# Optimization experiments

Hardware: AMD Instinct MI355X
Metric: run time of the kernel (lower is better)

The kernel has to match this reference:

```python
import jax, jax.numpy as jnp
import numpy as np

B, S, D = 2, 4096, 1024
H = 16
HD = D // H  # head_dim = 64

def setup_inputs() -> dict:
    key = jax.random.key(0)
    ks = jax.random.split(key, 9)
    sc = 1.0 / np.sqrt(D)
    return {
        "X":   jax.random.normal(ks[0], (B, S, D), dtype=jnp.float32),
        "Wq":  jax.random.normal(ks[1], (D, D), dtype=jnp.float32) * sc,
        "bq":  jax.random.normal(ks[2], (D,), dtype=jnp.float32) * 0.01,
        "Wk":  jax.random.normal(ks[3], (D, D), dtype=jnp.float32) * sc,
        "bk":  jax.random.normal(ks[4], (D,), dtype=jnp.float32) * 0.01,
        "Wv":  jax.random.normal(ks[5], (D, D), dtype=jnp.float32) * sc,
        "bv":  jax.random.normal(ks[6], (D,), dtype=jnp.float32) * 0.01,
        "Wo":  jax.random.normal(ks[7], (D, D), dtype=jnp.float32) * sc,
        "bo":  jax.random.normal(ks[8], (D,), dtype=jnp.float32) * 0.01,
    }

def reference(X, Wq, bq, Wk, bk, Wv, bv, Wo, bo):
    b, s, d = X.shape
    h, hd = H, HD
    # projections
    Q = X @ Wq + bq
    K = X @ Wk + bk
    V = X @ Wv + bv
    # [b, h, s, hd]
    Q = Q.reshape(b, s, h, hd).transpose(0, 2, 1, 3)
    K = K.reshape(b, s, h, hd).transpose(0, 2, 1, 3)
    V = V.reshape(b, s, h, hd).transpose(0, 2, 1, 3)
    scale = 1.0 / jnp.sqrt(jnp.asarray(hd, dtype=X.dtype))  # sqrt(hidden/num_heads)
    scores = jnp.einsum("bhqd,bhkd->bhqk", Q, K) * scale
    attn = jax.nn.softmax(scores, axis=-1)
    out = jnp.einsum("bhqk,bhkd->bhqd", attn, V)
    out = out.transpose(0, 2, 1, 3).reshape(b, s, d)
    return out @ Wo + bo
```

## Files before the change

kernel.cpp:

```cpp
#include <hip/hip_runtime.h>

#define Bsz 2
#define Sq  4096
#define Dm  1024
#define NH  16
#define HD  64

typedef __attribute__((ext_vector_type(8))) short short8;
typedef __attribute__((ext_vector_type(4))) float f32x4;
typedef __attribute__((ext_vector_type(2))) __fp16 fp16x2;
typedef __attribute__((ext_vector_type(4))) _Float16 half4v;
typedef __attribute__((ext_vector_type(8))) _Float16 half8v;

__device__ __forceinline__ unsigned short f2bf(float x) {
    unsigned int u = __float_as_uint(x);
    u += 0x7fffu + ((u >> 16) & 1u);
    return (unsigned short)(u >> 16);
}

__device__ __forceinline__ void gl2lds16(const unsigned short* g, unsigned short* l) {
    __builtin_amdgcn_global_load_lds(
        (const __attribute__((address_space(1))) unsigned int*)g,
        (__attribute__((address_space(3))) unsigned int*)l, 16, 0, 0);
}

__global__ __launch_bounds__(256) void cvt_bf16(const float4* __restrict__ in,
                                                ushort4* __restrict__ out) {
    const int i = blockIdx.x * 256 + threadIdx.x;
    const float4 v = in[i];
    ushort4 r;
    r.x = f2bf(v.x); r.y = f2bf(v.y); r.z = f2bf(v.z); r.w = f2bf(v.w);
    out[i] = r;
}

__global__ __launch_bounds__(256) void wtrans4(const float* __restrict__ Wq,
                                               const float* __restrict__ Wk,
                                               const float* __restrict__ Wv,
                                               const float* __restrict__ Wo,
                                               unsigned short* __restrict__ WtAll) {
    __shared__ float tile[64][65];
    const int z = blockIdx.z;
    const float* W = (z == 0) ? Wq : (z == 1) ? Wk : (z == 2) ? Wv : Wo;
    unsigned short* Wt = WtAll + (size_t)z * Dm * Dm;
    const int k0 = blockIdx.y * 64, n0 = blockIdx.x * 64;
    const int t = threadIdx.x;
    #pragma unroll
    for (int i = 0; i < 16; ++i) {
        const int idx = t + i * 256, r = idx >> 6, c = idx & 63;
        tile[r][c] = W[(size_t)(k0 + r) * Dm + n0 + c];
    }
    __syncthreads();
    #pragma unroll
    for (int i = 0; i < 16; ++i) {
        const int idx = t + i * 256, rr = idx >> 6, cc = idx & 63;
        Wt[(size_t)(n0 + rr) * Dm + k0 + cc] = f2bf(tile[cc][rr]);
    }
}

struct GemmCtx {
    int wm, wn, quad, c16;
    f32x4 acc[4][4];
};

__device__ __forceinline__ void gemm_core(
    const unsigned short* __restrict__ A,
    const unsigned short* __restrict__ Bt,
    int bm, int bn, unsigned short* As, unsigned short* Bs, GemmCtx& cx)
{
    const int t    = threadIdx.x;
    const int w    = t >> 6;
    const int lane = t & 63;
    cx.quad = lane >> 4;
    cx.c16  = lane & 15;
    cx.wm = (w >> 1) * 64;
    cx.wn = (w & 1) * 64;

    #pragma unroll
    for (int i = 0; i < 4; ++i)
        #pragma unroll
        for (int j = 0; j < 4; ++j)
            cx.acc[i][j] = (f32x4){0.f, 0.f, 0.f, 0.f};

    const int srow = lane >> 2, soff = (lane & 3) * 8;
    const unsigned short* Ag0 = A  + (size_t)(bm + w * 16 + srow) * Dm + soff;
    const unsigned short* Ag1 = Ag0 + (size_t)64 * Dm;
    const unsigned short* Bg0 = Bt + (size_t)(bn + w * 16 + srow) * Dm + soff;
    const unsigned short* Bg1 = Bg0 + (size_t)64 * Dm;
    unsigned short* Al0 = As + (w * 16) * 32;
    unsigned short* Al1 = As + (64 + w * 16) * 32;
    unsigned short* Bl0 = Bs + (w * 16) * 32;
    unsigned short* Bl1 = Bs + (64 + w * 16) * 32;

    for (int k0 = 0; k0 < Dm; k0 += 32) {
        __syncthreads();
        gl2lds16(Ag0 + k0, Al0);
        gl2lds16(Ag1 + k0, Al1);
        gl2lds16(Bg0 + k0, Bl0);
        gl2lds16(Bg1 + k0, Bl1);
        __syncthreads();

        short8 af[4], bf[4];
        #pragma unroll
        for (int mt = 0; mt < 4; ++mt)
            af[mt] = *(const short8*)(As + (cx.wm + mt * 16 + cx.c16) * 32 + cx.quad * 8);
        #pragma unroll
        for (int nt = 0; nt < 4; ++nt)
            bf[nt] = *(const short8*)(Bs + (cx.wn + nt * 16 + cx.c16) * 32 + cx.quad * 8);
        #pragma unroll
        for (int mt = 0; mt < 4; ++mt)
            #pragma unroll
            for (int nt = 0; nt < 4; ++nt)
                cx.acc[mt][nt] = __builtin_amdgcn_mfma_f32_16x16x32_bf16(
                    af[mt], bf[nt], cx.acc[mt][nt], 0, 0, 0);
    }
}

__global__ __launch_bounds__(256) void gemm_qkv(
    const unsigned short* __restrict__ A,
    const unsigned short* __restrict__ WtAll,
    const float* __restrict__ bq, const float* __restrict__ bk,
    const float* __restrict__ bv,
    unsigned short* __restrict__ Qh, unsigned short* __restrict__ Kh,
    unsigned short* __restrict__ Vt, float qscale)
{
    __shared__ unsigned short As[128 * 32];
    __shared__ unsigned short Bs[128 * 32];
    const int bm = blockIdx.y * 128;
    const int bn = blockIdx.x * 128;
    GemmCtx cx;
    gemm_core(A, WtAll, bm, bn, As, Bs, cx);

    const int which = bn >> 10;
    const float* bias = (which == 0) ? bq : (which == 1) ? bk : bv;
    const float osc = (which == 0) ? qscale : 1.0f;

    #pragma unroll
    for (int mt = 0; mt < 4; ++mt) {
        const int m0 = bm + cx.wm + mt * 16 + cx.quad * 4;
        #pragma unroll
        for (int nt = 0; nt < 4; ++nt) {
            const int n  = bn + cx.wn + nt * 16 + cx.c16;
            const int nl = n & 1023;
            const float bvv = bias[nl];
            const int h = (nl >> 6), d = nl & 63;
            if (which < 2) {
                unsigned short* C = (which == 0) ? Qh : Kh;
                #pragma unroll
                for (int r = 0; r < 4; ++r) {
                    const int m = m0 + r;
                    const int b = m >> 12, s = m & (Sq - 1);
                    C[((size_t)(b * NH + h) * Sq + s) * HD + d] =
                        f2bf((cx.acc[mt][nt][r] + bvv) * osc);
                }
            } else {
                const int b = m0 >> 12, s0 = m0 & (Sq - 1);
                union { fp16x2 h2[2]; unsigned int u[2]; } pk;
                pk.h2[0] = __builtin_amdgcn_cvt_pkrtz(cx.acc[mt][nt][0] + bvv,
                                                      cx.acc[mt][nt][1] + bvv);
                pk.h2[1] = __builtin_amdgcn_cvt_pkrtz(cx.acc[mt][nt][2] + bvv,
                                                      cx.acc[mt][nt][3] + bvv);
                *(uint2*)(Vt + ((size_t)(b * NH + h) * HD + d) * Sq + s0) =
                    make_uint2(pk.u[0], pk.u[1]);
            }
        }
    }
}

__global__ __launch_bounds__(256) void gemm_o(
    const unsigned short* __restrict__ A,
    const unsigned short* __restrict__ Bt,
    const float* __restrict__ bias, float* __restrict__ C)
{
    __shared__ unsigned short As[128 * 32];
    __shared__ unsigned short Bs[128 * 32];
    const int bm = blockIdx.y * 128;
    const int bn = blockIdx.x * 128;
    GemmCtx cx;
    gemm_core(A, Bt, bm, bn, As, Bs, cx);

    #pragma unroll
    for (int mt = 0; mt < 4; ++mt) {
        const int m0 = bm + cx.wm + mt * 16 + cx.quad * 4;
        #pragma unroll
        for (int nt = 0; nt < 4; ++nt) {
            const int n = bn + cx.wn + nt * 16 + cx.c16;
            const float bvv = bias[n];
            #pragma unroll
            for (int r = 0; r < 4; ++r)
                C[(size_t)(m0 + r) * Dm + n] = cx.acc[mt][nt][r] + bvv;
        }
    }
}

__global__ __launch_bounds__(256, 2) void attn_mfma6(
    const unsigned short* __restrict__ Q,
    const unsigned short* __restrict__ K,
    const unsigned short* __restrict__ Vt,
    unsigned short* __restrict__ AO)
{
    __shared__ unsigned short Ks[2][64 * 64];
    __shared__ unsigned short Vs[2][64 * 64];

    const int qt = blockIdx.x;
    const int bh = blockIdx.y;
    const int b = bh >> 4, h = bh & 15;
    const int t    = threadIdx.x;
    const int w    = t >> 6;
    const int lane = t & 63;
    const int quad = lane >> 4;
    const int c16  = lane & 15;
    const size_t base = (size_t)bh * Sq * HD;

    short8 qf[4][2];
    #pragma unroll
    for (int qg = 0; qg < 4; ++qg) {
        const unsigned short* qp =
            Q + base + (size_t)(qt * 256 + w * 64 + qg * 16 + c16) * HD;
        qf[qg][0] = *(const short8*)(qp + quad * 8);
        qf[qg][1] = *(const short8*)(qp + 32 + quad * 8);
    }

    f32x4 O[4][4];
    f32x4 Lsum[4];
    #pragma unroll
    for (int qg = 0; qg < 4; ++qg) {
        Lsum[qg] = (f32x4){0.f, 0.f, 0.f, 0.f};
        #pragma unroll
        for (int g = 0; g < 4; ++g)
            O[qg][g] = (f32x4){0.f, 0.f, 0.f, 0.f};
    }
    half8v ones8;
    #pragma unroll
    for (int i = 0; i < 8; ++i) ones8[i] = (_Float16)1.f;

    const int srow = t >> 2, sc4 = (t & 3) * 8;
    const int swr = (srow & 7) << 3;
    const int f0 = (sc4 < 16) ? sc4 * 2 : (sc4 - 16) * 2 + 4;
    const int f1 = (sc4 + 4 < 16) ? (sc4 + 4) * 2 : (sc4 - 12) * 2 + 4;
    const int kc0 = sc4 ^ swr, kc1 = (sc4 + 32) ^ swr;
    const int vc0 = f0 ^ swr, vc1 = f1 ^ swr;
    const int vc2 = (32 + f0) ^ swr, vc3 = (32 + f1) ^ swr;

    const unsigned short* kg = K  + base + (size_t)srow * HD + sc4;
    const unsigned short* vg = Vt + base + (size_t)srow * Sq + sc4;
    unsigned short* ksl = &Ks[0][0] + srow * 64;
    unsigned short* vsl = &Vs[0][0] + srow * 64;
    const int LBUF = 64 * 64;

    int4 kr0, kr1, vr0, vr1;
    kr0 = *(const int4*)(kg);
    kr1 = *(const int4*)(kg + 32);
    vr0 = *(const int4*)(vg);
    vr1 = *(const int4*)(vg + 32);
    *(int4*)(ksl + kc0) = kr0;
    *(int4*)(ksl + kc1) = kr1;
    *(uint2*)(vsl + vc0) = make_uint2(vr0.x, vr0.y);
    *(uint2*)(vsl + vc1) = make_uint2(vr0.z, vr0.w);
    *(uint2*)(vsl + vc2) = make_uint2(vr1.x, vr1.y);
    *(uint2*)(vsl + vc3) = make_uint2(vr1.z, vr1.w);

    for (int kt = 0; kt < Sq / 64; ++kt) {
        const int cur = kt & 1;
        if (kt + 1 < Sq / 64) {
            const unsigned short* kp = kg + (size_t)(kt + 1) * 64 * HD;
            const unsigned short* vp = vg + (kt + 1) * 64;
            kr0 = *(const int4*)(kp);
            kr1 = *(const int4*)(kp + 32);
            vr0 = *(const int4*)(vp);
            vr1 = *(const int4*)(vp + 32);
        }
        __syncthreads();

        const unsigned short* ksb = &Ks[cur][0];
        const unsigned short* vsb = &Vs[cur][0];

        half4v P4[4][4];
        #pragma unroll
        for (int nt = 0; nt < 4; ++nt) {
            const int krow = nt * 16 + c16;
            const int ksw = (krow & 7) << 3;
            const short8 kf0 = *(const short8*)(ksb + krow * 64 + ((quad * 8) ^ ksw));
            const short8 kf1 = *(const short8*)(ksb + krow * 64 + ((32 + quad * 8) ^ ksw));
            #pragma unroll
            for (int qg = 0; qg < 4; ++qg) {
                f32x4 z = (f32x4){0.f, 0.f, 0.f, 0.f};
                z = __builtin_amdgcn_mfma_f32_16x16x32_bf16(kf0, qf[qg][0], z, 0, 0, 0);
                z = __builtin_amdgcn_mfma_f32_16x16x32_bf16(kf1, qf[qg][1], z, 0, 0, 0);
                const float p0 = __builtin_amdgcn_exp2f(z[0]);
                const float p1 = __builtin_amdgcn_exp2f(z[1]);
                const float p2 = __builtin_amdgcn_exp2f(z[2]);
                const float p3 = __builtin_amdgcn_exp2f(z[3]);
                union { fp16x2 h2[2]; half4v h4; } pk;
                pk.h2[0] = __builtin_amdgcn_cvt_pkrtz(p0, p1);
                pk.h2[1] = __builtin_amdgcn_cvt_pkrtz(p2, p3);
                P4[qg][nt] = pk.h4;
            }
        }

        half8v P32[4][2];
        #pragma unroll
        for (int qg = 0; qg < 4; ++qg) {
            #pragma unroll
            for (int cc = 0; cc < 2; ++cc) {
                union { half4v h4[2]; half8v h8; } u;
                u.h4[0] = P4[qg][2 * cc];
                u.h4[1] = P4[qg][2 * cc + 1];
                P32[qg][cc] = u.h8;
            }
        }

        #pragma unroll
        for (int cc = 0; cc < 2; ++cc) {
            #pragma unroll
            for (int g = 0; g < 4; ++g) {
                const int vrow = g * 16 + c16;
                const half8v vf = *(const half8v*)
                    (vsb + vrow * 64 + ((cc * 32 + quad * 8) ^ ((vrow & 7) << 3)));
                #pragma unroll
                for (int qg = 0; qg < 4; ++qg)
                    O[qg][g] = __builtin_amdgcn_mfma_f32_16x16x32_f16(
                        P32[qg][cc], vf, O[qg][g], 0, 0, 0);
            }
            #pragma unroll
            for (int qg = 0; qg < 4; ++qg)
                Lsum[qg] = __builtin_amdgcn_mfma_f32_16x16x32_f16(
                    P32[qg][cc], ones8, Lsum[qg], 0, 0, 0);
        }

        if (kt + 1 < Sq / 64) {
            const int nb = cur ^ 1;
            *(int4*)(ksl + nb * LBUF + kc0) = kr0;
            *(int4*)(ksl + nb * LBUF + kc1) = kr1;
            unsigned short* vdst = vsl + nb * LBUF;
            *(uint2*)(vdst + vc0) = make_uint2(vr0.x, vr0.y);
            *(uint2*)(vdst + vc1) = make_uint2(vr0.z, vr0.w);
            *(uint2*)(vdst + vc2) = make_uint2(vr1.x, vr1.y);
            *(uint2*)(vdst + vc3) = make_uint2(vr1.z, vr1.w);
        }
    }

    #pragma unroll
    for (int qg = 0; qg < 4; ++qg) {
        float linv[4];
        #pragma unroll
        for (int r = 0; r < 4; ++r) linv[r] = 1.f / Lsum[qg][r];
        #pragma unroll
        for (int g = 0; g < 4; ++g) {
            const int col = h * HD + g * 16 + c16;
            #pragma unroll
            for (int r = 0; r < 4; ++r) {
                const int s = qt * 256 + w * 64 + qg * 16 + quad * 4 + r;
                AO[((size_t)(b * Sq + s)) * Dm + col] = f2bf(O[qg][g][r] * linv[r]);
            }
        }
    }
}

extern "C" void kernel_launch(void* const* d_in, const int* in_sizes, int n_in,
                              void* d_out, int out_size, void* d_ws, size_t ws_size,
                              hipStream_t stream)
{
    const float* X  = (const float*)d_in[0];
    const float* Wq = (const float*)d_in[1];
    const float* bq = (const float*)d_in[2];
    const float* Wk = (const float*)d_in[3];
    const float* bk = (const float*)d_in[4];
    const float* Wv = (const float*)d_in[5];
    const float* bv = (const float*)d_in[6];
    const float* Wo = (const float*)d_in[7];
    const float* bo = (const float*)d_in[8];
    float* out = (float*)d_out;

    unsigned short* ws = (unsigned short*)d_ws;
    const size_t NX = (size_t)Bsz * Sq * Dm;
    const size_t NW = (size_t)Dm * Dm;
    unsigned short* Xb    = ws; ws += NX;
    unsigned short* WtAll = ws; ws += 4 * NW;
    unsigned short* Qh    = ws; ws += NX;
    unsigned short* Kh    = ws; ws += NX;
    unsigned short* Vt    = ws; ws += NX;
    unsigned short* AO    = ws; ws += NX;

    cvt_bf16<<<(int)(NX / 1024), 256, 0, stream>>>((const float4*)X, (ushort4*)Xb);
    wtrans4<<<dim3(16, 16, 4), 256, 0, stream>>>(Wq, Wk, Wv, Wo, WtAll);

    const float SCL = 0.18033688011112042f;
    gemm_qkv<<<dim3(3 * Dm / 128, (Bsz * Sq) / 128), 256, 0, stream>>>(
        Xb, WtAll, bq, bk, bv, Qh, Kh, Vt, SCL);

    attn_mfma6<<<dim3(Sq / 256, Bsz * NH), 256, 0, stream>>>(Qh, Kh, Vt, AO);

    gemm_o<<<dim3(Dm / 128, (Bsz * Sq) / 128), 256, 0, stream>>>(
        AO, WtAll + 3 * NW, bo, out);
}
```

Measured before the change: 319.0 us.

## Halve attention query tile, raise occupancy, remap grid, add MFMA priority hints

The attention kernel now covers 128 query rows per workgroup instead of 256, which doubles the grid to 1024 workgroups. Launch bounds rise to 4 blocks per CU, and a 1D block index is remapped so neighbouring workgroups are spread across heads, likely to balance L2 reuse of K/V across XCDs. s_setprio raises wave priority around the MFMA sections so matrix work from one wave can overlap exp work from others. Each K/V tile loaded into LDS is now reused by fewer queries, so total K/V traffic doubles in exchange for more waves to hide latency.

```diff
diff --git a/kernel.cpp b/kernel.cpp
--- a/kernel.cpp
+++ b/kernel.cpp
@@ -192,7 +192,7 @@
     }
 }
 
-__global__ __launch_bounds__(256, 2) void attn_mfma6(
+__global__ __launch_bounds__(256, 4) void attn_mfma7(
     const unsigned short* __restrict__ Q,
     const unsigned short* __restrict__ K,
     const unsigned short* __restrict__ Vt,
@@ -201,8 +201,10 @@
     __shared__ unsigned short Ks[2][64 * 64];
     __shared__ unsigned short Vs[2][64 * 64];
 
-    const int qt = blockIdx.x;
-    const int bh = blockIdx.y;
+    const int wg  = blockIdx.x;
+    const int j   = wg >> 3;
+    const int bh  = (wg & 7) * 4 + (j >> 5);
+    const int qt  = j & 31;
     const int b = bh >> 4, h = bh & 15;
     const int t    = threadIdx.x;
     const int w    = t >> 6;
@@ -211,19 +213,19 @@
     const int c16  = lane & 15;
     const size_t base = (size_t)bh * Sq * HD;
 
-    short8 qf[4][2];
-    #pragma unroll
-    for (int qg = 0; qg < 4; ++qg) {
+    short8 qf[2][2];
+    #pragma unroll
+    for (int qg = 0; qg < 2; ++qg) {
         const unsigned short* qp =
-            Q + base + (size_t)(qt * 256 + w * 64 + qg * 16 + c16) * HD;
+            Q + base + (size_t)(qt * 128 + w * 32 + qg * 16 + c16) * HD;
         qf[qg][0] = *(const short8*)(qp + quad * 8);
         qf[qg][1] = *(const short8*)(qp + 32 + quad * 8);
     }
 
-    f32x4 O[4][4];
-    f32x4 Lsum[4];
-    #pragma unroll
-    for (int qg = 0; qg < 4; ++qg) {
+    f32x4 O[2][4];
+    f32x4 Lsum[2];
+    #pragma unroll
+    for (int qg = 0; qg < 2; ++qg) {
         Lsum[qg] = (f32x4){0.f, 0.f, 0.f, 0.f};
         #pragma unroll
         for (int g = 0; g < 4; ++g)
@@ -274,22 +276,28 @@
         const unsigned short* ksb = &Ks[cur][0];
         const unsigned short* vsb = &Vs[cur][0];
 
-        half4v P4[4][4];
+        half4v P4[2][4];
         #pragma unroll
         for (int nt = 0; nt < 4; ++nt) {
             const int krow = nt * 16 + c16;
             const int ksw = (krow & 7) << 3;
             const short8 kf0 = *(const short8*)(ksb + krow * 64 + ((quad * 8) ^ ksw));
             const short8 kf1 = *(const short8*)(ksb + krow * 64 + ((32 + quad * 8) ^ ksw));
-            #pragma unroll
-            for (int qg = 0; qg < 4; ++qg) {
-                f32x4 z = (f32x4){0.f, 0.f, 0.f, 0.f};
-                z = __builtin_amdgcn_mfma_f32_16x16x32_bf16(kf0, qf[qg][0], z, 0, 0, 0);
-                z = __builtin_amdgcn_mfma_f32_16x16x32_bf16(kf1, qf[qg][1], z, 0, 0, 0);
-                const float p0 = __builtin_amdgcn_exp2f(z[0]);
-                const float p1 = __builtin_amdgcn_exp2f(z[1]);
-                const float p2 = __builtin_amdgcn_exp2f(z[2]);
-                const float p3 = __builtin_amdgcn_exp2f(z[3]);
+            f32x4 z[2];
+            __builtin_amdgcn_s_setprio(1);
+            #pragma unroll
+            for (int qg = 0; qg < 2; ++qg) {
+                z[qg] = (f32x4){0.f, 0.f, 0.f, 0.f};
+                z[qg] = __builtin_amdgcn_mfma_f32_16x16x32_bf16(kf0, qf[qg][0], z[qg], 0, 0, 0);
+                z[qg] = __builtin_amdgcn_mfma_f32_16x16x32_bf16(kf1, qf[qg][1], z[qg], 0, 0, 0);
+            }
+            __builtin_amdgcn_s_setprio(0);
+            #pragma unroll
+            for (int qg = 0; qg < 2; ++qg) {
+                const float p0 = __builtin_amdgcn_exp2f(z[qg][0]);
+                const float p1 = __builtin_amdgcn_exp2f(z[qg][1]);
+                const float p2 = __builtin_amdgcn_exp2f(z[qg][2]);
+                const float p3 = __builtin_amdgcn_exp2f(z[qg][3]);
                 union { fp16x2 h2[2]; half4v h4; } pk;
                 pk.h2[0] = __builtin_amdgcn_cvt_pkrtz(p0, p1);
                 pk.h2[1] = __builtin_amdgcn_cvt_pkrtz(p2, p3);
@@ -297,9 +305,9 @@
             }
         }
 
-        half8v P32[4][2];
-        #pragma unroll
-        for (int qg = 0; qg < 4; ++qg) {
+        half8v P32[2][2];
+        #pragma unroll
+        for (int qg = 0; qg < 2; ++qg) {
             #pragma unroll
             for (int cc = 0; cc < 2; ++cc) {
                 union { half4v h4[2]; half8v h8; } u;
@@ -309,6 +317,7 @@
             }
         }
 
+        __builtin_amdgcn_s_setprio(1);
         #pragma unroll
         for (int cc = 0; cc < 2; ++cc) {
             #pragma unroll
@@ -317,15 +326,16 @@
                 const half8v vf = *(const half8v*)
                     (vsb + vrow * 64 + ((cc * 32 + quad * 8) ^ ((vrow & 7) << 3)));
                 #pragma unroll
-                for (int qg = 0; qg < 4; ++qg)
+                for (int qg = 0; qg < 2; ++qg)
                     O[qg][g] = __builtin_amdgcn_mfma_f32_16x16x32_f16(
                         P32[qg][cc], vf, O[qg][g], 0, 0, 0);
             }
             #pragma unroll
-            for (int qg = 0; qg < 4; ++qg)
+            for (int qg = 0; qg < 2; ++qg)
                 Lsum[qg] = __builtin_amdgcn_mfma_f32_16x16x32_f16(
                     P32[qg][cc], ones8, Lsum[qg], 0, 0, 0);
         }
+        __builtin_amdgcn_s_setprio(0);
 
         if (kt + 1 < Sq / 64) {
             const int nb = cur ^ 1;
@@ -340,7 +350,7 @@
     }
 
     #pragma unroll
-    for (int qg = 0; qg < 4; ++qg) {
+    for (int qg = 0; qg < 2; ++qg) {
         float linv[4];
         #pragma unroll
         for (int r = 0; r < 4; ++r) linv[r] = 1.f / Lsum[qg][r];
@@ -349,7 +359,7 @@
             const int col = h * HD + g * 16 + c16;
             #pragma unroll
             for (int r = 0; r < 4; ++r) {
-                const int s = qt * 256 + w * 64 + qg * 16 + quad * 4 + r;
+                const int s = qt * 128 + w * 32 + qg * 16 + quad * 4 + r;
                 AO[((size_t)(b * Sq + s)) * Dm + col] = f2bf(O[qg][g][r] * linv[r]);
             }
         }
@@ -388,7 +398,7 @@
     gemm_qkv<<<dim3(3 * Dm / 128, (Bsz * Sq) / 128), 256, 0, stream>>>(
         Xb, WtAll, bq, bk, bv, Qh, Kh, Vt, SCL);
 
-    attn_mfma6<<<dim3(Sq / 256, Bsz * NH), 256, 0, stream>>>(Qh, Kh, Vt, AO);
+    attn_mfma7<<<dim3(32 * 32), 256, 0, stream>>>(Qh, Kh, Vt, AO);
 
     gemm_o<<<dim3(Dm / 128, (Bsz * Sq) / 128), 256, 0, stream>>>(
         AO, WtAll + 3 * NW, bo, out);
```

Measured after the change: 345.8 us. 1.08x slower.

## Software-pipeline QK MFMA with exp and remap attention grid for XCD locality

Applied to the files above, without the earlier changes.

Restructures the attention inner loop so the QK^T MFMAs for one 16-key slice are issued while the exp2/convert work of the previous slice runs. Sched barriers and s_setprio around the MFMA groups enforce that interleaving, and the K/V LDS stores for the next tile are split around the two PV steps. It also flattens the grid to one dimension and remaps block IDs so that consecutive blocks (wg & 7 selecting the XCD) map to a fixed set of batch-heads, aiming for better L2 reuse of K/V. The cost is more live registers for the z buffers, which could affect occupancy at 2 waves per SIMD.

```diff
diff --git a/kernel.cpp b/kernel.cpp
--- a/kernel.cpp
+++ b/kernel.cpp
@@ -192,7 +192,7 @@
     }
 }
 
-__global__ __launch_bounds__(256, 2) void attn_mfma6(
+__global__ __launch_bounds__(256, 2) void attn_mfma8(
     const unsigned short* __restrict__ Q,
     const unsigned short* __restrict__ K,
     const unsigned short* __restrict__ Vt,
@@ -201,8 +201,10 @@
     __shared__ unsigned short Ks[2][64 * 64];
     __shared__ unsigned short Vs[2][64 * 64];
 
-    const int qt = blockIdx.x;
-    const int bh = blockIdx.y;
+    const int wg  = blockIdx.x;
+    const int j   = wg >> 3;
+    const int bh  = (wg & 7) * 4 + (j >> 4);
+    const int qt  = j & 15;
     const int b = bh >> 4, h = bh & 15;
     const int t    = threadIdx.x;
     const int w    = t >> 6;
@@ -274,63 +276,83 @@
         const unsigned short* ksb = &Ks[cur][0];
         const unsigned short* vsb = &Vs[cur][0];
 
+        f32x4 z0[4], z1[4], z2[4], z3[4];
         half4v P4[4][4];
-        #pragma unroll
-        for (int nt = 0; nt < 4; ++nt) {
-            const int krow = nt * 16 + c16;
+
+        auto qkstep = [&](int nt5, f32x4* z) {
+            const int krow = nt5 * 16 + c16;
             const int ksw = (krow & 7) << 3;
             const short8 kf0 = *(const short8*)(ksb + krow * 64 + ((quad * 8) ^ ksw));
             const short8 kf1 = *(const short8*)(ksb + krow * 64 + ((32 + quad * 8) ^ ksw));
+            __builtin_amdgcn_s_setprio(1);
             #pragma unroll
             for (int qg = 0; qg < 4; ++qg) {
-                f32x4 z = (f32x4){0.f, 0.f, 0.f, 0.f};
-                z = __builtin_amdgcn_mfma_f32_16x16x32_bf16(kf0, qf[qg][0], z, 0, 0, 0);
-                z = __builtin_amdgcn_mfma_f32_16x16x32_bf16(kf1, qf[qg][1], z, 0, 0, 0);
-                const float p0 = __builtin_amdgcn_exp2f(z[0]);
-                const float p1 = __builtin_amdgcn_exp2f(z[1]);
-                const float p2 = __builtin_amdgcn_exp2f(z[2]);
-                const float p3 = __builtin_amdgcn_exp2f(z[3]);
+                f32x4 zz = (f32x4){0.f, 0.f, 0.f, 0.f};
+                zz = __builtin_amdgcn_mfma_f32_16x16x32_bf16(kf0, qf[qg][0], zz, 0, 0, 0);
+                zz = __builtin_amdgcn_mfma_f32_16x16x32_bf16(kf1, qf[qg][1], zz, 0, 0, 0);
+                z[qg] = zz;
+            }
+            __builtin_amdgcn_s_setprio(0);
+            __builtin_amdgcn_sched_barrier(0);
+        };
+        auto expstep = [&](const f32x4* z, half4v* Pn) {
+            #pragma unroll
+            for (int qg = 0; qg < 4; ++qg) {
+                const float p0 = __builtin_amdgcn_exp2f(z[qg][0]);
+                const float p1 = __builtin_amdgcn_exp2f(z[qg][1]);
+                const float p2 = __builtin_amdgcn_exp2f(z[qg][2]);
+                const float p3 = __builtin_amdgcn_exp2f(z[qg][3]);
                 union { fp16x2 h2[2]; half4v h4; } pk;
                 pk.h2[0] = __builtin_amdgcn_cvt_pkrtz(p0, p1);
                 pk.h2[1] = __builtin_amdgcn_cvt_pkrtz(p2, p3);
-                P4[qg][nt] = pk.h4;
-            }
-        }
-
-        half8v P32[4][2];
-        #pragma unroll
-        for (int qg = 0; qg < 4; ++qg) {
-            #pragma unroll
-            for (int cc = 0; cc < 2; ++cc) {
+                Pn[qg] = pk.h4;
+            }
+        };
+        auto pvstep = [&](int cc) {
+            half8v P32[4];
+            #pragma unroll
+            for (int qg = 0; qg < 4; ++qg) {
                 union { half4v h4[2]; half8v h8; } u;
-                u.h4[0] = P4[qg][2 * cc];
-                u.h4[1] = P4[qg][2 * cc + 1];
-                P32[qg][cc] = u.h8;
-            }
-        }
-
-        #pragma unroll
-        for (int cc = 0; cc < 2; ++cc) {
+                u.h4[0] = P4[2 * cc][qg];
+                u.h4[1] = P4[2 * cc + 1][qg];
+                P32[qg] = u.h8;
+            }
+            half8v vf[4];
             #pragma unroll
             for (int g = 0; g < 4; ++g) {
                 const int vrow = g * 16 + c16;
-                const half8v vf = *(const half8v*)
+                vf[g] = *(const half8v*)
                     (vsb + vrow * 64 + ((cc * 32 + quad * 8) ^ ((vrow & 7) << 3)));
+            }
+            __builtin_amdgcn_s_setprio(1);
+            #pragma unroll
+            for (int g = 0; g < 4; ++g)
                 #pragma unroll
                 for (int qg = 0; qg < 4; ++qg)
                     O[qg][g] = __builtin_amdgcn_mfma_f32_16x16x32_f16(
-                        P32[qg][cc], vf, O[qg][g], 0, 0, 0);
-            }
+                        P32[qg], vf[g], O[qg][g], 0, 0, 0);
             #pragma unroll
             for (int qg = 0; qg < 4; ++qg)
                 Lsum[qg] = __builtin_amdgcn_mfma_f32_16x16x32_f16(
-                    P32[qg][cc], ones8, Lsum[qg], 0, 0, 0);
-        }
-
+                    P32[qg], ones8, Lsum[qg], 0, 0, 0);
+            __builtin_amdgcn_s_setprio(0);
+            __builtin_amdgcn_sched_barrier(0);
+        };
+
+        qkstep(0, z0);
+        qkstep(1, z1);  expstep(z0, P4[0]);
+        qkstep(2, z2);  expstep(z1, P4[1]);
+        qkstep(3, z3);  expstep(z2, P4[2]);
+        pvstep(0);
+        expstep(z3, P4[3]);
         if (kt + 1 < Sq / 64) {
             const int nb = cur ^ 1;
             *(int4*)(ksl + nb * LBUF + kc0) = kr0;
             *(int4*)(ksl + nb * LBUF + kc1) = kr1;
+        }
+        pvstep(1);
+        if (kt + 1 < Sq / 64) {
+            const int nb = cur ^ 1;
             unsigned short* vdst = vsl + nb * LBUF;
             *(uint2*)(vdst + vc0) = make_uint2(vr0.x, vr0.y);
             *(uint2*)(vdst + vc1) = make_uint2(vr0.z, vr0.w);
@@ -388,7 +410,7 @@
     gemm_qkv<<<dim3(3 * Dm / 128, (Bsz * Sq) / 128), 256, 0, stream>>>(
         Xb, WtAll, bq, bk, bv, Qh, Kh, Vt, SCL);
 
-    attn_mfma6<<<dim3(Sq / 256, Bsz * NH), 256, 0, stream>>>(Qh, Kh, Vt, AO);
+    attn_mfma8<<<dim3(512), 256, 0, stream>>>(Qh, Kh, Vt, AO);
 
     gemm_o<<<dim3(Dm / 128, (Bsz * Sq) / 128), 256, 0, stream>>>(
         AO, WtAll + 3 * NW, bo, out);
```

Result: no change. 316.7 us (-0.7%).

## Async K loads to LDS, remap blocks across XCDs, and reorder MFMA with setprio

Applied to the files above, without the earlier changes.

The attention kernel now loads K tiles straight into LDS with global_load_lds, so K no longer passes through registers. The 1D grid is remapped so consecutive workgroups, which land on different XCDs, each take a different (batch, head), which should improve L2 reuse of K/V. The S=QK^T MFMAs are regrouped per K subtile, V fragments are prefetched, and the PV MFMAs are split in two halves around the V LDS store. s_setprio is added around MFMA bursts to encourage overlap across waves. The barrier moves to the top of the loop, which is still correct under double buffering but reorders the synchronisation.

```diff
diff --git a/kernel.cpp b/kernel.cpp
--- a/kernel.cpp
+++ b/kernel.cpp
@@ -192,7 +192,7 @@
     }
 }
 
-__global__ __launch_bounds__(256, 2) void attn_mfma6(
+__global__ __launch_bounds__(256, 2) void attn_mfma11(
     const unsigned short* __restrict__ Q,
     const unsigned short* __restrict__ K,
     const unsigned short* __restrict__ Vt,
@@ -201,8 +201,10 @@
     __shared__ unsigned short Ks[2][64 * 64];
     __shared__ unsigned short Vs[2][64 * 64];
 
-    const int qt = blockIdx.x;
-    const int bh = blockIdx.y;
+    const int wg  = blockIdx.x;
+    const int j   = wg >> 3;
+    const int bh  = (wg & 7) * 4 + (j >> 4);
+    const int qt  = j & 15;
     const int b = bh >> 4, h = bh & 15;
     const int t    = threadIdx.x;
     const int w    = t >> 6;
@@ -232,28 +234,27 @@
     half8v ones8;
     #pragma unroll
     for (int i = 0; i < 8; ++i) ones8[i] = (_Float16)1.f;
+    const f32x4 zero4 = (f32x4){0.f, 0.f, 0.f, 0.f};
+
+    const int lrow = lane >> 3, lchunk = lane & 7;
+    const unsigned short* kgA = K + base + (size_t)(16 * w + lrow) * HD
+                                  + (lchunk ^ lrow) * 8;
+    unsigned short* klA = &Ks[0][0] + (16 * w) * 64;
+    const int LBUF = 64 * 64;
 
     const int srow = t >> 2, sc4 = (t & 3) * 8;
     const int swr = (srow & 7) << 3;
     const int f0 = (sc4 < 16) ? sc4 * 2 : (sc4 - 16) * 2 + 4;
     const int f1 = (sc4 + 4 < 16) ? (sc4 + 4) * 2 : (sc4 - 12) * 2 + 4;
-    const int kc0 = sc4 ^ swr, kc1 = (sc4 + 32) ^ swr;
     const int vc0 = f0 ^ swr, vc1 = f1 ^ swr;
     const int vc2 = (32 + f0) ^ swr, vc3 = (32 + f1) ^ swr;
-
-    const unsigned short* kg = K  + base + (size_t)srow * HD + sc4;
     const unsigned short* vg = Vt + base + (size_t)srow * Sq + sc4;
-    unsigned short* ksl = &Ks[0][0] + srow * 64;
     unsigned short* vsl = &Vs[0][0] + srow * 64;
-    const int LBUF = 64 * 64;
-
-    int4 kr0, kr1, vr0, vr1;
-    kr0 = *(const int4*)(kg);
-    kr1 = *(const int4*)(kg + 32);
-    vr0 = *(const int4*)(vg);
-    vr1 = *(const int4*)(vg + 32);
-    *(int4*)(ksl + kc0) = kr0;
-    *(int4*)(ksl + kc1) = kr1;
+
+    gl2lds16(kgA, klA);
+    gl2lds16(kgA + (size_t)8 * HD, klA + 8 * 64);
+    int4 vr0 = *(const int4*)(vg);
+    int4 vr1 = *(const int4*)(vg + 32);
     *(uint2*)(vsl + vc0) = make_uint2(vr0.x, vr0.y);
     *(uint2*)(vsl + vc1) = make_uint2(vr0.z, vr0.w);
     *(uint2*)(vsl + vc2) = make_uint2(vr1.x, vr1.y);
@@ -261,82 +262,116 @@
 
     for (int kt = 0; kt < Sq / 64; ++kt) {
         const int cur = kt & 1;
-        if (kt + 1 < Sq / 64) {
-            const unsigned short* kp = kg + (size_t)(kt + 1) * 64 * HD;
+        const int nb = cur ^ 1;
+        const bool pre = (kt + 1 < Sq / 64);
+        __syncthreads();
+
+        if (pre) {
+            const unsigned short* kp = kgA + (size_t)(kt + 1) * 64 * HD;
+            gl2lds16(kp, klA + nb * LBUF);
+            gl2lds16(kp + (size_t)8 * HD, klA + nb * LBUF + 8 * 64);
             const unsigned short* vp = vg + (kt + 1) * 64;
-            kr0 = *(const int4*)(kp);
-            kr1 = *(const int4*)(kp + 32);
             vr0 = *(const int4*)(vp);
             vr1 = *(const int4*)(vp + 32);
         }
-        __syncthreads();
 
         const unsigned short* ksb = &Ks[cur][0];
         const unsigned short* vsb = &Vs[cur][0];
 
-        half4v P4[4][4];
+        short8 kf[4][2];
         #pragma unroll
         for (int nt = 0; nt < 4; ++nt) {
             const int krow = nt * 16 + c16;
             const int ksw = (krow & 7) << 3;
-            const short8 kf0 = *(const short8*)(ksb + krow * 64 + ((quad * 8) ^ ksw));
-            const short8 kf1 = *(const short8*)(ksb + krow * 64 + ((32 + quad * 8) ^ ksw));
+            kf[nt][0] = *(const short8*)(ksb + krow * 64 + ((quad * 8) ^ ksw));
+            kf[nt][1] = *(const short8*)(ksb + krow * 64 + ((32 + quad * 8) ^ ksw));
+        }
+        half8v vfa[4];
+        #pragma unroll
+        for (int g = 0; g < 4; ++g) {
+            const int vrow = g * 16 + c16;
+            vfa[g] = *(const half8v*)
+                (vsb + vrow * 64 + ((quad * 8) ^ ((vrow & 7) << 3)));
+        }
+
+        half4v P4[4][4];
+        #pragma unroll
+        for (int nt = 0; nt < 4; ++nt) {
+            f32x4 z[4];
+            __builtin_amdgcn_s_setprio(1);
+            #pragma unroll
+            for (int qg = 0; qg < 4; ++qg)
+                z[qg] = __builtin_amdgcn_mfma_f32_16x16x32_bf16(
+                    kf[nt][0], qf[qg][0], zero4, 0, 0, 0);
+            #pragma unroll
+            for (int qg = 0; qg < 4; ++qg)
+                z[qg] = __builtin_amdgcn_mfma_f32_16x16x32_bf16(
+                    kf[nt][1], qf[qg][1], z[qg], 0, 0, 0);
+            __builtin_amdgcn_s_setprio(0);
             #pragma unroll
             for (int qg = 0; qg < 4; ++qg) {
-                f32x4 z = (f32x4){0.f, 0.f, 0.f, 0.f};
-                z = __builtin_amdgcn_mfma_f32_16x16x32_bf16(kf0, qf[qg][0], z, 0, 0, 0);
-                z = __builtin_amdgcn_mfma_f32_16x16x32_bf16(kf1, qf[qg][1], z, 0, 0, 0);
-                const float p0 = __builtin_amdgcn_exp2f(z[0]);
-                const float p1 = __builtin_amdgcn_exp2f(z[1]);
-                const float p2 = __builtin_amdgcn_exp2f(z[2]);
-                const float p3 = __builtin_amdgcn_exp2f(z[3]);
+                const float p0 = __builtin_amdgcn_exp2f(z[qg][0]);
+                const float p1 = __builtin_amdgcn_exp2f(z[qg][1]);
+                const float p2 = __builtin_amdgcn_exp2f(z[qg][2]);
+                const float p3 = __builtin_amdgcn_exp2f(z[qg][3]);
                 union { fp16x2 h2[2]; half4v h4; } pk;
                 pk.h2[0] = __builtin_amdgcn_cvt_pkrtz(p0, p1);
                 pk.h2[1] = __builtin_amdgcn_cvt_pkrtz(p2, p3);
-                P4[qg][nt] = pk.h4;
+                P4[nt][qg] = pk.h4;
             }
         }
 
-        half8v P32[4][2];
+        half8v vfb[4];
+        #pragma unroll
+        for (int g = 0; g < 4; ++g) {
+            const int vrow = g * 16 + c16;
+            vfb[g] = *(const half8v*)
+                (vsb + vrow * 64 + ((32 + quad * 8) ^ ((vrow & 7) << 3)));
+        }
+
+        half8v P32a[4], P32b[4];
         #pragma unroll
         for (int qg = 0; qg < 4; ++qg) {
-            #pragma unroll
-            for (int cc = 0; cc < 2; ++cc) {
-                union { half4v h4[2]; half8v h8; } u;
-                u.h4[0] = P4[qg][2 * cc];
-                u.h4[1] = P4[qg][2 * cc + 1];
-                P32[qg][cc] = u.h8;
-            }
-        }
-
-        #pragma unroll
-        for (int cc = 0; cc < 2; ++cc) {
-            #pragma unroll
-            for (int g = 0; g < 4; ++g) {
-                const int vrow = g * 16 + c16;
-                const half8v vf = *(const half8v*)
-                    (vsb + vrow * 64 + ((cc * 32 + quad * 8) ^ ((vrow & 7) << 3)));
-                #pragma unroll
-                for (int qg = 0; qg < 4; ++qg)
-                    O[qg][g] = __builtin_amdgcn_mfma_f32_16x16x32_f16(
-                        P32[qg][cc], vf, O[qg][g], 0, 0, 0);
-            }
+            union { half4v h4[2]; half8v h8; } ua, ub;
+            ua.h4[0] = P4[0][qg];  ua.h4[1] = P4[1][qg];
+            ub.h4[0] = P4[2][qg];  ub.h4[1] = P4[3][qg];
+            P32a[qg] = ua.h8;
+            P32b[qg] = ub.h8;
+        }
+
+        __builtin_amdgcn_s_setprio(1);
+        #pragma unroll
+        for (int g = 0; g < 4; ++g)
             #pragma unroll
             for (int qg = 0; qg < 4; ++qg)
-                Lsum[qg] = __builtin_amdgcn_mfma_f32_16x16x32_f16(
-                    P32[qg][cc], ones8, Lsum[qg], 0, 0, 0);
-        }
-
-        if (kt + 1 < Sq / 64) {
-            const int nb = cur ^ 1;
-            *(int4*)(ksl + nb * LBUF + kc0) = kr0;
-            *(int4*)(ksl + nb * LBUF + kc1) = kr1;
+                O[qg][g] = __builtin_amdgcn_mfma_f32_16x16x32_f16(
+                    P32a[qg], vfa[g], O[qg][g], 0, 0, 0);
+        #pragma unroll
+        for (int qg = 0; qg < 4; ++qg)
+            Lsum[qg] = __builtin_amdgcn_mfma_f32_16x16x32_f16(
+                P32a[qg], ones8, Lsum[qg], 0, 0, 0);
+        __builtin_amdgcn_s_setprio(0);
+
+        if (pre) {
             unsigned short* vdst = vsl + nb * LBUF;
             *(uint2*)(vdst + vc0) = make_uint2(vr0.x, vr0.y);
             *(uint2*)(vdst + vc1) = make_uint2(vr0.z, vr0.w);
             *(uint2*)(vdst + vc2) = make_uint2(vr1.x, vr1.y);
             *(uint2*)(vdst + vc3) = make_uint2(vr1.z, vr1.w);
         }
+
+        __builtin_amdgcn_s_setprio(1);
+        #pragma unroll
+        for (int g = 0; g < 4; ++g)
+            #pragma unroll
+            for (int qg = 0; qg < 4; ++qg)
+                O[qg][g] = __builtin_amdgcn_mfma_f32_16x16x32_f16(
+                    P32b[qg], vfb[g], O[qg][g], 0, 0, 0);
+        #pragma unroll
+        for (int qg = 0; qg < 4; ++qg)
+            Lsum[qg] = __builtin_amdgcn_mfma_f32_16x16x32_f16(
+                P32b[qg], ones8, Lsum[qg], 0, 0, 0);
+        __builtin_amdgcn_s_setprio(0);
     }
 
     #pragma unroll
@@ -388,7 +423,7 @@
     gemm_qkv<<<dim3(3 * Dm / 128, (Bsz * Sq) / 128), 256, 0, stream>>>(
         Xb, WtAll, bq, bk, bv, Qh, Kh, Vt, SCL);
 
-    attn_mfma6<<<dim3(Sq / 256, Bsz * NH), 256, 0, stream>>>(Qh, Kh, Vt, AO);
+    attn_mfma11<<<dim3(512), 256, 0, stream>>>(Qh, Kh, Vt, AO);
 
     gemm_o<<<dim3(Dm / 128, (Bsz * Sq) / 128), 256, 0, stream>>>(
         AO, WtAll + 3 * NW, bo, out);
```

After: 325.6 us. 2.1% more time.
